# Optimization experiments

Hardware: AMD Instinct MI355X
Metric: run time of the kernel (lower is better)

The kernel has to match this reference:

```python
import math
import jax, jax.numpy as jnp
import numpy as np

B, T, C = 8, 1024, 512
H = 8
NUM_FRAMES = 128  # num_tokens
NUM_ANIMALS = 8   # num_id; NUM_FRAMES * NUM_ANIMALS == T


def _linear_params(key, fan_in, fan_out):
    kw, kb = jax.random.split(key)
    bound = 1.0 / math.sqrt(fan_in)
    W = jax.random.uniform(kw, (fan_out, fan_in), jnp.float32, -bound, bound)
    b = jax.random.uniform(kb, (fan_out,), jnp.float32, -bound, bound)
    return W, b


def setup_inputs() -> dict:
    key = jax.random.key(0)
    ks = jax.random.split(key, 6)
    x = jax.random.normal(ks[0], (B, T, C), jnp.float32)
    mask = jnp.ones((B, T), jnp.float32)
    Wq, bq = _linear_params(ks[1], C, C)
    Wk, bk = _linear_params(ks[2], C, C)
    Wv, bv = _linear_params(ks[3], C, C)
    Wp, bp = _linear_params(ks[4], C, C)
    return {"x": x, "mask": mask, "Wq": Wq, "bq": bq, "Wk": Wk, "bk": bk,
            "Wv": Wv, "bv": bv, "Wp": Wp, "bp": bp}


def _block_causal_mask():
    # tril over frames, expanded so all animals within a frame attend to all
    # animals of frames <= current frame: kron(tril(F,F), ones(I,I)) -> (T,T)
    tril = jnp.tril(jnp.ones((NUM_FRAMES, NUM_FRAMES), jnp.float32))
    return jnp.kron(tril, jnp.ones((NUM_ANIMALS, NUM_ANIMALS), jnp.float32))


def reference(x, mask, Wq, bq, Wk, bk, Wv, bv, Wp, bp):
    Bx, Tx, Cx = x.shape
    d = Cx // H
    q = (x @ Wq.T + bq).reshape(Bx, Tx, H, d).transpose(0, 2, 1, 3)  # b h t d
    k = (x @ Wk.T + bk).reshape(Bx, Tx, H, d).transpose(0, 2, 1, 3)
    v = (x @ Wv.T + bv).reshape(Bx, Tx, H, d).transpose(0, 2, 1, 3)
    att = jnp.einsum('bhqd,bhkd->bhqk', q, k) * (1.0 / math.sqrt(d))
    m = _block_causal_mask()[None, None] * mask[:, None, None, :]  # (B,1,T,T)
    att = jnp.where(m == 0, -jnp.inf, att)
    att = jax.nn.softmax(att, axis=-1)
    # dropout is identity (pdrop=0.0 / eval mode)
    y = jnp.einsum('bhqk,bhkd->bhqd', att, v)
    y = y.transpose(0, 2, 1, 3).reshape(Bx, Tx, Cx)
    return y @ Wp.T + bp
```

## Files before the change

kernel.cpp:

```cpp
#include <hip/hip_runtime.h>
#include <cstdint>
#include <cstddef>

#define BB 8
#define TT 1024
#define CC 512
#define HH 8
#define DD 64
#define MM (BB*TT)

typedef short s16x4 __attribute__((ext_vector_type(4)));
typedef _Float16 f16x8 __attribute__((ext_vector_type(8)));
typedef float f32x4  __attribute__((ext_vector_type(4)));
typedef unsigned u32x4 __attribute__((ext_vector_type(4)));

__device__ __forceinline__ short f2hs(float f) {
  _Float16 h = (_Float16)f;
  return __builtin_bit_cast(short, h);
}
__device__ __forceinline__ unsigned pkh(float a, float b) {
  return __builtin_bit_cast(unsigned, __builtin_amdgcn_cvt_pkrtz(a, b));
}

__device__ __forceinline__ f32x4 mfma16h(f16x8 a, f16x8 b, f32x4 c) {
  return __builtin_amdgcn_mfma_f32_16x16x32_f16(a, b, c, 0, 0, 0);
}

__device__ __forceinline__ void gload_lds16(const void* g, void* l) {
  __builtin_amdgcn_global_load_lds(
      (const __attribute__((address_space(1))) unsigned int*)g,
      (__attribute__((address_space(3))) unsigned int*)l, 16, 0, 0);
}

__global__ void prep_kernel(const float* __restrict__ x,
                            const float* __restrict__ mask,
                            const float* __restrict__ Wq,
                            const float* __restrict__ Wk,
                            const float* __restrict__ Wv,
                            const float* __restrict__ Wp,
                            short* __restrict__ Xh,
                            short* __restrict__ Wqkv,
                            short* __restrict__ Wpc,
                            float* __restrict__ maskAdd) {
  const int NXv = MM * CC / 4;
  const int NWv = CC * CC / 4;
  const int NM = BB * TT;
  int stride = gridDim.x * blockDim.x;
  for (int i = blockIdx.x * blockDim.x + threadIdx.x; i < NXv + 4 * NWv + NM; i += stride) {
    if (i < NXv) {
      int e = i * 4;
      float4 v = *(const float4*)(x + e);
      s16x4 h = {f2hs(v.x), f2hs(v.y), f2hs(v.z), f2hs(v.w)};
      *(s16x4*)(Xh + e) = h;
    } else if (i < NXv + 4 * NWv) {
      int wi = i - NXv;
      int wsel = wi >> 16;
      int idx = wi & 65535;
      int r = idx >> 7, c = (idx & 127) << 2;
      const float* W = (wsel == 0) ? Wq : (wsel == 1) ? Wk : (wsel == 2) ? Wv : Wp;
      float4 v = *(const float4*)(W + (size_t)r * CC + c);
      s16x4 h = {f2hs(v.x), f2hs(v.y), f2hs(v.z), f2hs(v.w)};
      short* dst = (wsel < 3) ? (Wqkv + (size_t)(wsel * 512 + r) * CC + c)
                              : (Wpc + (size_t)r * CC + c);
      *(s16x4*)dst = h;
    } else {
      int mi = i - NXv - 4 * NWv;
      maskAdd[mi] = (mask[mi] == 0.f) ? -1e30f : 0.f;
    }
  }
}

template <int BN, int EPI>
__global__ __launch_bounds__(512, 4) void gemm_kernel(
    const short* __restrict__ A, const short* __restrict__ Bw,
    const float* __restrict__ b0, const float* __restrict__ b1,
    const float* __restrict__ b2,
    short* __restrict__ qo, short* __restrict__ ko, short* __restrict__ vt,
    float* __restrict__ outp) {
  constexpr int MR = 4;
  constexpr int NR = BN / 64;
  constexpr int ABYT = 128 * 128;
  constexpr int TILE = ABYT + BN * 128;
  constexpr int NT = 8;
  constexpr int BL = BN / 64;
  __shared__ __align__(1024) char smem[2 * TILE];

  const int tid = threadIdx.x;
  const int lane = tid & 63;
  const int w = tid >> 6;
  const int wm = w >> 2, wn = w & 3;
  const int l15 = lane & 15, lg = lane >> 4;
  const int lsw = (l15 & 7) << 4;
  const int sr8 = lane >> 3;
  const int scbsw = ((lane & 7) * 16) ^ (sr8 << 4);

  const int rowA = blockIdx.x * 128;
  const int rowB = blockIdx.y * BN;
  const char* Ab = (const char*)A + (size_t)(rowA + sr8) * 1024 + scbsw;
  const char* Bb = (const char*)Bw + (size_t)(rowB + sr8) * 1024 + scbsw;

  f32x4 acc[MR][NR] = {};

  auto STAGE_A = [&](char* dst, int kt) {
#pragma unroll
    for (int g = 0; g < 2; ++g) {
      int r0 = (w * 2 + g) * 8;
      gload_lds16(Ab + (size_t)r0 * 1024 + (size_t)kt * 128, dst + r0 * 128);
    }
  };
  auto STAGE_B = [&](char* dst, int kt) {
#pragma unroll
    for (int g = 0; g < BL; ++g) {
      int r0 = (w * BL + g) * 8;
      gload_lds16(Bb + (size_t)r0 * 1024 + (size_t)kt * 128, dst + ABYT + r0 * 128);
    }
  };
  auto RDA2 = [&](const char* buf, int mh, int kk, f16x8* af) {
#pragma unroll
    for (int i = 0; i < 2; ++i) {
      int row = wm * 64 + (mh * 2 + i) * 16 + l15;
      af[i] = *(const f16x8*)(buf + row * 128 + ((kk * 64 + lg * 16) ^ lsw));
    }
  };
  auto RDBk = [&](const char* buf, int kk, f16x8* bfr) {
#pragma unroll
    for (int j = 0; j < NR; ++j) {
      int row = wn * (BN / 4) + j * 16 + l15;
      bfr[j] = *(const f16x8*)(buf + ABYT + row * 128 + ((kk * 64 + lg * 16) ^ lsw));
    }
  };

  STAGE_A(smem, 0);
  STAGE_B(smem, 0);
  asm volatile("s_waitcnt vmcnt(0)" ::: "memory");
  __builtin_amdgcn_s_barrier();

  for (int t = 0; t < NT; ++t) {
    char* bufp = smem + (t & 1) * TILE;
    char* bufn = smem + ((t + 1) & 1) * TILE;
    f16x8 af[2], bfr[NR];

#define PH(MH)                                                                \
  __builtin_amdgcn_s_barrier();                                               \
  asm volatile("s_waitcnt lgkmcnt(0)" ::: "memory");                          \
  __builtin_amdgcn_sched_barrier(0);                                          \
  __builtin_amdgcn_s_setprio(1);                                              \
  _Pragma("unroll")                                                           \
  for (int i = 0; i < 2; ++i)                                                 \
    _Pragma("unroll")                                                         \
    for (int j = 0; j < NR; ++j)                                              \
      acc[(MH) * 2 + i][j] = mfma16h(af[i], bfr[j], acc[(MH) * 2 + i][j]);    \
  __builtin_amdgcn_s_setprio(0);

    RDBk(bufp, 0, bfr);
    RDA2(bufp, 0, 0, af);
    if (t + 1 < NT) STAGE_A(bufn, t + 1);
    PH(0)
    RDA2(bufp, 1, 0, af);
    if (t + 1 < NT) STAGE_B(bufn, t + 1);
    PH(1)
    RDBk(bufp, 1, bfr);
    RDA2(bufp, 1, 1, af);
    PH(1)
    RDA2(bufp, 0, 1, af);
    PH(0)
#undef PH
    asm volatile("s_waitcnt vmcnt(0)" ::: "memory");
    __builtin_amdgcn_s_barrier();
  }

#pragma unroll
  for (int m = 0; m < MR; ++m) {
    int rbase = rowA + wm * 64 + m * 16 + lg * 4;
#pragma unroll
    for (int n = 0; n < NR; ++n) {
      int col = rowB + wn * (BN / 4) + n * 16 + l15;
#pragma unroll
      for (int j = 0; j < 4; ++j) {
        float v = acc[m][n][j];
        int r = rbase + j;
        if constexpr (EPI == 0) {
          int b = r >> 10, t = r & 1023;
          int wsel = col >> 9, c = col & 511;
          int h = c >> 6, dd = c & 63;
          int bh = b * HH + h;
          if (wsel == 0) {
            qo[((size_t)bh * TT + t) * DD + dd] = f2hs((v + b0[c]) * 0.125f);
          } else if (wsel == 1) {
            ko[((size_t)bh * TT + t) * DD + dd] = f2hs(v + b1[c]);
          } else {
            vt[((size_t)bh * DD + dd) * TT + t] = f2hs(v + b2[c]);
          }
        } else {
          outp[(size_t)r * CC + col] = v + b0[col];
        }
      }
    }
  }
}

__global__ __launch_bounds__(256, 4) void attn_kernel(
    const short* __restrict__ q, const short* __restrict__ k,
    const short* __restrict__ vt, const float* __restrict__ maskAdd,
    short* __restrict__ Yh) {
  const int blk = blockIdx.x;
  const int k4 = blk >> 8;
  const int r = blk & 255;
  const int bh = r >> 2;
  const int j4 = r & 3;
  const int qb = (k4 & 1) ? ((k4 & 2) ? (4 + j4) : j4)
                          : ((k4 & 2) ? (11 - j4) : (15 - j4));
  const int b = bh >> 3, h = bh & 7;
  const int tid = threadIdx.x;
  const int lane = tid & 63;
  const int w = tid >> 6;
  const int l15 = lane & 15, lg = lane >> 4;
  const int lsw = (l15 & 7) << 4;

  __shared__ short Ks[2][64 * 64];
  __shared__ short Vs[2][64 * 64];

  const short* kbh = k + (size_t)bh * TT * DD;
  const short* vbh = vt + (size_t)bh * DD * TT;

  const int sr32 = tid >> 3;
  const int scb = (tid & 7) * 16;

  auto STAGE = [&](int bs, int tile) {
#pragma unroll
    for (int g = 0; g < 2; ++g) {
      int row = g * 32 + sr32;
      int sw = (row & 7) << 4;
      gload_lds16((const char*)kbh + ((size_t)tile * 64 + row) * 128 + (scb ^ sw),
                  (char*)&Ks[bs][0] + row * 128);
      gload_lds16((const char*)vbh + (size_t)row * 2048 + tile * 128 + (scb ^ sw),
                  (char*)&Vs[bs][0] + row * 128);
    }
  };

  const int qrow = qb * 64 + w * 16 + l15;
  const short* qptr = q + ((size_t)bh * TT + qrow) * DD;
  f16x8 qf0 = *(const f16x8*)(qptr + lg * 8);
  f16x8 qf1 = *(const f16x8*)(qptr + 32 + lg * 8);

  f32x4 yacc[4] = {};
  float mrun = -1e30f, lpart = 0.f;

  const int srcA = (((2 * lg) & 3) << 4) + l15;
  const int srcB = (((2 * lg + 1) & 3) << 4) + l15;
  const bool hiSel = (lg >= 2);

  STAGE(0, 0);
  __syncthreads();

  int buf = 0;
  for (int jt = 0; jt <= qb; ++jt) {
    if (jt < qb) STAGE(buf ^ 1, jt + 1);

    f32x4 sacc[4];
#pragma unroll
    for (int n = 0; n < 4; ++n)
      sacc[n] = *(const f32x4*)(maskAdd + (size_t)b * TT + jt * 64 + n * 16 + lg * 4);
    __builtin_amdgcn_s_setprio(1);
#pragma unroll
    for (int c = 0; c < 2; ++c) {
      f16x8 qc = (c == 0) ? qf0 : qf1;
#pragma unroll
      for (int n = 0; n < 4; ++n) {
        int krow = n * 16 + l15;
        const f16x8 kf = *(const f16x8*)((const char*)&Ks[buf][0] + krow * 128 + ((c * 64 + lg * 16) ^ lsw));
        sacc[n] = mfma16h(kf, qc, sacc[n]);
      }
    }
    __builtin_amdgcn_s_setprio(0);
    if (jt == qb) {
      const int qloc8 = (w * 16 + l15) >> 3;
#pragma unroll
      for (int n = 0; n < 4; ++n)
#pragma unroll
        for (int jj = 0; jj < 4; ++jj) {
          int kloc = n * 16 + lg * 4 + jj;
          if ((kloc >> 3) > qloc8) sacc[n][jj] = -1e30f;
        }
    }
    float t0 = fmaxf(fmaxf(sacc[0][0], sacc[0][1]), fmaxf(sacc[0][2], sacc[0][3]));
    float t1 = fmaxf(fmaxf(sacc[1][0], sacc[1][1]), fmaxf(sacc[1][2], sacc[1][3]));
    float t2 = fmaxf(fmaxf(sacc[2][0], sacc[2][1]), fmaxf(sacc[2][2], sacc[2][3]));
    float t3 = fmaxf(fmaxf(sacc[3][0], sacc[3][1]), fmaxf(sacc[3][2], sacc[3][3]));
    float pmL = fmaxf(fmaxf(t0, t1), fmaxf(t2, t3));
    if (!__all(pmL <= mrun + 8.0f)) {
      float pm = fmaxf(pmL, __shfl_xor(pmL, 16));
      pm = fmaxf(pm, __shfl_xor(pm, 32));
      float mnew = fmaxf(mrun, pm);
      float alpha = __expf(mrun - mnew);
      mrun = mnew;
      lpart *= alpha;
      float ab[4];
#pragma unroll
      for (int jj = 0; jj < 4; ++jj) ab[jj] = __shfl(alpha, lg * 4 + jj);
#pragma unroll
      for (int dt = 0; dt < 4; ++dt)
#pragma unroll
        for (int jj = 0; jj < 4; ++jj) yacc[dt][jj] *= ab[jj];
    }
    unsigned pk2[4][2];
    float lps = 0.f;
#pragma unroll
    for (int n = 0; n < 4; ++n) {
      float p0 = __expf(sacc[n][0] - mrun);
      float p1 = __expf(sacc[n][1] - mrun);
      float p2 = __expf(sacc[n][2] - mrun);
      float p3 = __expf(sacc[n][3] - mrun);
      lps += (p0 + p1) + (p2 + p3);
      pk2[n][0] = pkh(p0, p1);
      pk2[n][1] = pkh(p2, p3);
    }
    lpart += lps;
    f16x8 pa[2];
#pragma unroll
    for (int c = 0; c < 2; ++c) {
      unsigned a0 = __shfl(pk2[2 * c][0], srcA);
      unsigned a1 = __shfl(pk2[2 * c][1], srcA);
      unsigned a2 = __shfl(pk2[2 * c][0], srcB);
      unsigned a3 = __shfl(pk2[2 * c][1], srcB);
      unsigned b0 = __shfl(pk2[2 * c + 1][0], srcA);
      unsigned b1 = __shfl(pk2[2 * c + 1][1], srcA);
      unsigned b2 = __shfl(pk2[2 * c + 1][0], srcB);
      unsigned b3 = __shfl(pk2[2 * c + 1][1], srcB);
      u32x4 tv = {hiSel ? b0 : a0, hiSel ? b1 : a1, hiSel ? b2 : a2, hiSel ? b3 : a3};
      pa[c] = __builtin_bit_cast(f16x8, tv);
    }
    __builtin_amdgcn_s_setprio(1);
#pragma unroll
    for (int c = 0; c < 2; ++c) {
#pragma unroll
      for (int dt = 0; dt < 4; ++dt) {
        int vrow = dt * 16 + l15;
        const f16x8 vf = *(const f16x8*)((const char*)&Vs[buf][0] + vrow * 128 + ((c * 64 + lg * 16) ^ lsw));
        yacc[dt] = mfma16h(pa[c], vf, yacc[dt]);
      }
    }
    __builtin_amdgcn_s_setprio(0);

    __syncthreads();
    buf ^= 1;
  }

  float lr = lpart;
  lr += __shfl_xor(lr, 16);
  lr += __shfl_xor(lr, 32);
  float lb[4];
#pragma unroll
  for (int jj = 0; jj < 4; ++jj) lb[jj] = 1.f / __shfl(lr, lg * 4 + jj);
#pragma unroll
  for (int dt = 0; dt < 4; ++dt) {
    int col = h * DD + dt * 16 + l15;
#pragma unroll
    for (int jj = 0; jj < 4; ++jj) {
      int row = b * TT + qb * 64 + w * 16 + lg * 4 + jj;
      float y = yacc[dt][jj] * lb[jj];
      Yh[(size_t)row * CC + col] = f2hs(y);
    }
  }
}

extern "C" void kernel_launch(void* const* d_in, const int* in_sizes, int n_in,
                              void* d_out, int out_size, void* d_ws, size_t ws_size,
                              hipStream_t stream) {
  const float* x    = (const float*)d_in[0];
  const float* mask = (const float*)d_in[1];
  const float* Wq   = (const float*)d_in[2];
  const float* bq   = (const float*)d_in[3];
  const float* Wk   = (const float*)d_in[4];
  const float* bk   = (const float*)d_in[5];
  const float* Wv   = (const float*)d_in[6];
  const float* bv   = (const float*)d_in[7];
  const float* Wp   = (const float*)d_in[8];
  const float* bp   = (const float*)d_in[9];
  float* out = (float*)d_out;

  char* ws = (char*)d_ws;
  short* Xh   = (short*)(ws);
  short* Wqkv = (short*)(ws + (size_t)8 * 1048576);
  short* Wpc  = (short*)(ws + (size_t)10 * 1048576);
  short* qo   = (short*)(ws + (size_t)11 * 1048576);
  short* ko   = (short*)(ws + (size_t)19 * 1048576);
  short* vt   = (short*)(ws + (size_t)27 * 1048576);
  short* Yh   = (short*)(ws + (size_t)35 * 1048576);
  float* maskAdd = (float*)(ws + (size_t)43 * 1048576);

  prep_kernel<<<2048, 256, 0, stream>>>(x, mask, Wq, Wk, Wv, Wp, Xh, Wqkv, Wpc, maskAdd);

  gemm_kernel<192, 0><<<dim3(64, 8), 512, 0, stream>>>(
      Xh, Wqkv, bq, bk, bv, qo, ko, vt, nullptr);

  attn_kernel<<<dim3(1024), 256, 0, stream>>>(qo, ko, vt, maskAdd, Yh);

  gemm_kernel<64, 1><<<dim3(64, 8), 512, 0, stream>>>(
      Yh, Wpc, bp, nullptr, nullptr, nullptr, nullptr, nullptr, out);
}
```

Before: 73.99 us.

## Fuse attention and output projection with grid barrier; retile QKV GEMM

Merges the attention and output-projection kernels into one persistent 512-block kernel. Each block runs two (batch, head) attention units, then all blocks meet at a global atomic barrier before doing the projection GEMM. The QKV GEMM moves to 96-wide N tiles on a 64x16 grid so more blocks run, and the barrier counters are reset in the prep kernel. This removes one kernel launch and the launch gap, but the spin barrier assumes all 512 blocks are resident at once and adds a synchronisation stall.

```diff
diff --git a/kernel.cpp b/kernel.cpp
--- a/kernel.cpp
+++ b/kernel.cpp
@@ -41,7 +41,9 @@
                             short* __restrict__ Xh,
                             short* __restrict__ Wqkv,
                             short* __restrict__ Wpc,
-                            float* __restrict__ maskAdd) {
+                            float* __restrict__ maskAdd,
+                            unsigned* __restrict__ bar) {
+  if (blockIdx.x == 0 && threadIdx.x == 0) { bar[0] = 0u; bar[1] = 0u; }
   const int NXv = MM * CC / 4;
   const int NWv = CC * CC / 4;
   const int NM = BB * TT;
@@ -70,32 +72,29 @@
   }
 }
 
-template <int BN, int EPI>
-__global__ __launch_bounds__(512, 4) void gemm_kernel(
+__global__ __launch_bounds__(512, 4) void qkv_kernel(
     const short* __restrict__ A, const short* __restrict__ Bw,
     const float* __restrict__ b0, const float* __restrict__ b1,
     const float* __restrict__ b2,
-    short* __restrict__ qo, short* __restrict__ ko, short* __restrict__ vt,
-    float* __restrict__ outp) {
-  constexpr int MR = 4;
-  constexpr int NR = BN / 64;
-  constexpr int ABYT = 128 * 128;
-  constexpr int TILE = ABYT + BN * 128;
+    short* __restrict__ qo, short* __restrict__ ko, short* __restrict__ vt) {
+  constexpr int MR = 2, NR = 3;
+  constexpr int ABYT = 16384;
+  constexpr int BBYT = 96 * 128;
+  constexpr int TILE = ABYT + BBYT;
   constexpr int NT = 8;
-  constexpr int BL = BN / 64;
   __shared__ __align__(1024) char smem[2 * TILE];
 
   const int tid = threadIdx.x;
   const int lane = tid & 63;
   const int w = tid >> 6;
-  const int wm = w >> 2, wn = w & 3;
+  const int wm = w >> 1, wn = w & 1;
   const int l15 = lane & 15, lg = lane >> 4;
   const int lsw = (l15 & 7) << 4;
   const int sr8 = lane >> 3;
   const int scbsw = ((lane & 7) * 16) ^ (sr8 << 4);
 
   const int rowA = blockIdx.x * 128;
-  const int rowB = blockIdx.y * BN;
+  const int rowB = blockIdx.y * 96;
   const char* Ab = (const char*)A + (size_t)(rowA + sr8) * 1024 + scbsw;
   const char* Bb = (const char*)Bw + (size_t)(rowB + sr8) * 1024 + scbsw;
 
@@ -109,23 +108,24 @@
     }
   };
   auto STAGE_B = [&](char* dst, int kt) {
-#pragma unroll
-    for (int g = 0; g < BL; ++g) {
-      int r0 = (w * BL + g) * 8;
-      gload_lds16(Bb + (size_t)r0 * 1024 + (size_t)kt * 128, dst + ABYT + r0 * 128);
+    int r0 = w * 8;
+    gload_lds16(Bb + (size_t)r0 * 1024 + (size_t)kt * 128, dst + ABYT + r0 * 128);
+    if (w < 4) {
+      int r1 = (8 + w) * 8;
+      gload_lds16(Bb + (size_t)r1 * 1024 + (size_t)kt * 128, dst + ABYT + r1 * 128);
     }
   };
-  auto RDA2 = [&](const char* buf, int mh, int kk, f16x8* af) {
-#pragma unroll
-    for (int i = 0; i < 2; ++i) {
-      int row = wm * 64 + (mh * 2 + i) * 16 + l15;
+  auto RDA = [&](const char* buf, int kk, f16x8* af) {
+#pragma unroll
+    for (int i = 0; i < MR; ++i) {
+      int row = wm * 32 + i * 16 + l15;
       af[i] = *(const f16x8*)(buf + row * 128 + ((kk * 64 + lg * 16) ^ lsw));
     }
   };
-  auto RDBk = [&](const char* buf, int kk, f16x8* bfr) {
+  auto RDB = [&](const char* buf, int kk, f16x8* bfr) {
 #pragma unroll
     for (int j = 0; j < NR; ++j) {
-      int row = wn * (BN / 4) + j * 16 + l15;
+      int row = wn * 48 + j * 16 + l15;
       bfr[j] = *(const f16x8*)(buf + ABYT + row * 128 + ((kk * 64 + lg * 16) ^ lsw));
     }
   };
@@ -138,228 +138,338 @@
   for (int t = 0; t < NT; ++t) {
     char* bufp = smem + (t & 1) * TILE;
     char* bufn = smem + ((t + 1) & 1) * TILE;
-    f16x8 af[2], bfr[NR];
-
-#define PH(MH)                                                                \
+    f16x8 af[MR], bfr[NR];
+
+    RDB(bufp, 0, bfr);
+    RDA(bufp, 0, af);
+    if (t + 1 < NT) STAGE_A(bufn, t + 1);
+    __builtin_amdgcn_s_barrier();
+    asm volatile("s_waitcnt lgkmcnt(0)" ::: "memory");
+    __builtin_amdgcn_sched_barrier(0);
+    __builtin_amdgcn_s_setprio(1);
+#pragma unroll
+    for (int i = 0; i < MR; ++i)
+#pragma unroll
+      for (int j = 0; j < NR; ++j)
+        acc[i][j] = mfma16h(af[i], bfr[j], acc[i][j]);
+    __builtin_amdgcn_s_setprio(0);
+
+    RDB(bufp, 1, bfr);
+    RDA(bufp, 1, af);
+    if (t + 1 < NT) STAGE_B(bufn, t + 1);
+    __builtin_amdgcn_s_barrier();
+    asm volatile("s_waitcnt lgkmcnt(0)" ::: "memory");
+    __builtin_amdgcn_sched_barrier(0);
+    __builtin_amdgcn_s_setprio(1);
+#pragma unroll
+    for (int i = 0; i < MR; ++i)
+#pragma unroll
+      for (int j = 0; j < NR; ++j)
+        acc[i][j] = mfma16h(af[i], bfr[j], acc[i][j]);
+    __builtin_amdgcn_s_setprio(0);
+
+    asm volatile("s_waitcnt vmcnt(0)" ::: "memory");
+    __builtin_amdgcn_s_barrier();
+  }
+
+#pragma unroll
+  for (int m = 0; m < MR; ++m) {
+    int rbase = rowA + wm * 32 + m * 16 + lg * 4;
+#pragma unroll
+    for (int n = 0; n < NR; ++n) {
+      int col = rowB + wn * 48 + n * 16 + l15;
+#pragma unroll
+      for (int j = 0; j < 4; ++j) {
+        float v = acc[m][n][j];
+        int r = rbase + j;
+        int b = r >> 10, t = r & 1023;
+        int wsel = col >> 9, c = col & 511;
+        int h = c >> 6, dd = c & 63;
+        int bh = b * HH + h;
+        if (wsel == 0) {
+          qo[((size_t)bh * TT + t) * DD + dd] = f2hs((v + b0[c]) * 0.125f);
+        } else if (wsel == 1) {
+          ko[((size_t)bh * TT + t) * DD + dd] = f2hs(v + b1[c]);
+        } else {
+          vt[((size_t)bh * DD + dd) * TT + t] = f2hs(v + b2[c]);
+        }
+      }
+    }
+  }
+}
+
+__global__ __launch_bounds__(512, 4) void attnproj_kernel(
+    const short* __restrict__ q, const short* __restrict__ k,
+    const short* __restrict__ vt, const float* __restrict__ maskAdd,
+    short* __restrict__ Yh, const short* __restrict__ Wpc,
+    const float* __restrict__ bp, float* __restrict__ out,
+    unsigned* __restrict__ bar) {
+  __shared__ __align__(1024) char smem[65536];
+
+  const int blk = blockIdx.x;
+  const int tid = threadIdx.x;
+
+  {
+    const int half = blk >> 8;
+    const int lin = blk & 255;
+    const int qb = half ? (15 - (lin >> 5)) : (lin >> 5);
+    const int bhp = lin & 31;
+    const int w8 = tid >> 6;
+    const int u = w8 >> 2;
+    const int w = w8 & 3;
+    const int bh = bhp * 2 + u;
+    const int b = bh >> 3, h = bh & 7;
+    const int lane = tid & 63;
+    const int l15 = lane & 15, lg = lane >> 4;
+    const int lsw = (l15 & 7) << 4;
+
+    char* KsU = smem + u * 32768;
+
+    const short* kbh = k + (size_t)bh * TT * DD;
+    const short* vbh = vt + (size_t)bh * DD * TT;
+
+    const int utid = tid & 255;
+    const int sr32 = utid >> 3;
+    const int scb = (utid & 7) * 16;
+
+    auto STAGE = [&](int bs, int tile) {
+#pragma unroll
+      for (int g = 0; g < 2; ++g) {
+        int row = g * 32 + sr32;
+        int sw = (row & 7) << 4;
+        gload_lds16((const char*)kbh + ((size_t)tile * 64 + row) * 128 + (scb ^ sw),
+                    KsU + bs * 8192 + row * 128);
+        gload_lds16((const char*)vbh + (size_t)row * 2048 + tile * 128 + (scb ^ sw),
+                    KsU + 16384 + bs * 8192 + row * 128);
+      }
+    };
+
+    const int qrow = qb * 64 + w * 16 + l15;
+    const short* qptr = q + ((size_t)bh * TT + qrow) * DD;
+    f16x8 qf0 = *(const f16x8*)(qptr + lg * 8);
+    f16x8 qf1 = *(const f16x8*)(qptr + 32 + lg * 8);
+
+    f32x4 yacc[4] = {};
+    float mrun = -1e30f, lpart = 0.f;
+
+    const int srcA = (((2 * lg) & 3) << 4) + l15;
+    const int srcB = (((2 * lg + 1) & 3) << 4) + l15;
+    const bool hiSel = (lg >= 2);
+
+    STAGE(0, 0);
+    __syncthreads();
+
+    int buf = 0;
+    for (int jt = 0; jt <= qb; ++jt) {
+      if (jt < qb) STAGE(buf ^ 1, jt + 1);
+
+      f32x4 sacc[4];
+#pragma unroll
+      for (int n = 0; n < 4; ++n)
+        sacc[n] = *(const f32x4*)(maskAdd + (size_t)b * TT + jt * 64 + n * 16 + lg * 4);
+      __builtin_amdgcn_s_setprio(1);
+#pragma unroll
+      for (int c = 0; c < 2; ++c) {
+        f16x8 qc = (c == 0) ? qf0 : qf1;
+#pragma unroll
+        for (int n = 0; n < 4; ++n) {
+          int krow = n * 16 + l15;
+          const f16x8 kf = *(const f16x8*)(KsU + buf * 8192 + krow * 128 + ((c * 64 + lg * 16) ^ lsw));
+          sacc[n] = mfma16h(kf, qc, sacc[n]);
+        }
+      }
+      __builtin_amdgcn_s_setprio(0);
+      if (jt == qb) {
+        const int qloc8 = (w * 16 + l15) >> 3;
+#pragma unroll
+        for (int n = 0; n < 4; ++n)
+#pragma unroll
+          for (int jj = 0; jj < 4; ++jj) {
+            int kloc = n * 16 + lg * 4 + jj;
+            if ((kloc >> 3) > qloc8) sacc[n][jj] = -1e30f;
+          }
+      }
+      float t0 = fmaxf(fmaxf(sacc[0][0], sacc[0][1]), fmaxf(sacc[0][2], sacc[0][3]));
+      float t1 = fmaxf(fmaxf(sacc[1][0], sacc[1][1]), fmaxf(sacc[1][2], sacc[1][3]));
+      float t2 = fmaxf(fmaxf(sacc[2][0], sacc[2][1]), fmaxf(sacc[2][2], sacc[2][3]));
+      float t3 = fmaxf(fmaxf(sacc[3][0], sacc[3][1]), fmaxf(sacc[3][2], sacc[3][3]));
+      float pmL = fmaxf(fmaxf(t0, t1), fmaxf(t2, t3));
+      if (!__all(pmL <= mrun + 8.0f)) {
+        float pm = fmaxf(pmL, __shfl_xor(pmL, 16));
+        pm = fmaxf(pm, __shfl_xor(pm, 32));
+        float mnew = fmaxf(mrun, pm);
+        float alpha = __expf(mrun - mnew);
+        mrun = mnew;
+        lpart *= alpha;
+        float ab[4];
+#pragma unroll
+        for (int jj = 0; jj < 4; ++jj) ab[jj] = __shfl(alpha, lg * 4 + jj);
+#pragma unroll
+        for (int dt = 0; dt < 4; ++dt)
+#pragma unroll
+          for (int jj = 0; jj < 4; ++jj) yacc[dt][jj] *= ab[jj];
+      }
+      unsigned pk2[4][2];
+      float lps = 0.f;
+#pragma unroll
+      for (int n = 0; n < 4; ++n) {
+        float p0 = __expf(sacc[n][0] - mrun);
+        float p1 = __expf(sacc[n][1] - mrun);
+        float p2 = __expf(sacc[n][2] - mrun);
+        float p3 = __expf(sacc[n][3] - mrun);
+        lps += (p0 + p1) + (p2 + p3);
+        pk2[n][0] = pkh(p0, p1);
+        pk2[n][1] = pkh(p2, p3);
+      }
+      lpart += lps;
+      f16x8 pa[2];
+#pragma unroll
+      for (int c = 0; c < 2; ++c) {
+        unsigned a0 = __shfl(pk2[2 * c][0], srcA);
+        unsigned a1 = __shfl(pk2[2 * c][1], srcA);
+        unsigned a2 = __shfl(pk2[2 * c][0], srcB);
+        unsigned a3 = __shfl(pk2[2 * c][1], srcB);
+        unsigned b0 = __shfl(pk2[2 * c + 1][0], srcA);
+        unsigned b1 = __shfl(pk2[2 * c + 1][1], srcA);
+        unsigned b2 = __shfl(pk2[2 * c + 1][0], srcB);
+        unsigned b3 = __shfl(pk2[2 * c + 1][1], srcB);
+        u32x4 tv = {hiSel ? b0 : a0, hiSel ? b1 : a1, hiSel ? b2 : a2, hiSel ? b3 : a3};
+        pa[c] = __builtin_bit_cast(f16x8, tv);
+      }
+      __builtin_amdgcn_s_setprio(1);
+#pragma unroll
+      for (int c = 0; c < 2; ++c) {
+#pragma unroll
+        for (int dt = 0; dt < 4; ++dt) {
+          int vrow = dt * 16 + l15;
+          const f16x8 vf = *(const f16x8*)(KsU + 16384 + buf * 8192 + vrow * 128 + ((c * 64 + lg * 16) ^ lsw));
+          yacc[dt] = mfma16h(pa[c], vf, yacc[dt]);
+        }
+      }
+      __builtin_amdgcn_s_setprio(0);
+
+      __syncthreads();
+      buf ^= 1;
+    }
+
+    float lr = lpart;
+    lr += __shfl_xor(lr, 16);
+    lr += __shfl_xor(lr, 32);
+    float lb[4];
+#pragma unroll
+    for (int jj = 0; jj < 4; ++jj) lb[jj] = 1.f / __shfl(lr, lg * 4 + jj);
+#pragma unroll
+    for (int dt = 0; dt < 4; ++dt) {
+      int col = h * DD + dt * 16 + l15;
+#pragma unroll
+      for (int jj = 0; jj < 4; ++jj) {
+        int row = b * TT + qb * 64 + w * 16 + lg * 4 + jj;
+        float y = yacc[dt][jj] * lb[jj];
+        Yh[(size_t)row * CC + col] = f2hs(y);
+      }
+    }
+  }
+
+  __syncthreads();
+  if (tid == 0) {
+    __threadfence();
+    if (atomicAdd(&bar[0], 1u) == 511u) {
+      atomicAdd(&bar[1], 1u);
+    } else {
+      while (atomicAdd(&bar[1], 0u) == 0u) __builtin_amdgcn_s_sleep(8);
+    }
+    __threadfence();
+  }
+  __syncthreads();
+
+  {
+    constexpr int ABYT = 16384;
+    constexpr int TILE = 24576;
+    constexpr int NT = 8;
+    const int bx = blk & 63, by = blk >> 6;
+    const int lane = tid & 63;
+    const int w = tid >> 6;
+    const int wm = w >> 2, wn = w & 3;
+    const int l15 = lane & 15, lg = lane >> 4;
+    const int lsw = (l15 & 7) << 4;
+    const int sr8 = lane >> 3;
+    const int scbsw = ((lane & 7) * 16) ^ (sr8 << 4);
+
+    const int rowA = bx * 128;
+    const int rowB = by * 64;
+    const char* Ab = (const char*)Yh + (size_t)(rowA + sr8) * 1024 + scbsw;
+    const char* Bb = (const char*)Wpc + (size_t)(rowB + sr8) * 1024 + scbsw;
+
+    f32x4 acc[4] = {};
+
+    auto STAGE_A = [&](char* dst, int kt) {
+#pragma unroll
+      for (int g = 0; g < 2; ++g) {
+        int r0 = (w * 2 + g) * 8;
+        gload_lds16(Ab + (size_t)r0 * 1024 + (size_t)kt * 128, dst + r0 * 128);
+      }
+    };
+    auto STAGE_B = [&](char* dst, int kt) {
+      int r0 = w * 8;
+      gload_lds16(Bb + (size_t)r0 * 1024 + (size_t)kt * 128, dst + ABYT + r0 * 128);
+    };
+    auto RDA2 = [&](const char* buf, int mh, int kk, f16x8* af) {
+#pragma unroll
+      for (int i = 0; i < 2; ++i) {
+        int row = wm * 64 + (mh * 2 + i) * 16 + l15;
+        af[i] = *(const f16x8*)(buf + row * 128 + ((kk * 64 + lg * 16) ^ lsw));
+      }
+    };
+    auto RDB1 = [&](const char* buf, int kk) {
+      int row = wn * 16 + l15;
+      return *(const f16x8*)(buf + ABYT + row * 128 + ((kk * 64 + lg * 16) ^ lsw));
+    };
+
+    STAGE_A(smem, 0);
+    STAGE_B(smem, 0);
+    asm volatile("s_waitcnt vmcnt(0)" ::: "memory");
+    __builtin_amdgcn_s_barrier();
+
+    for (int t = 0; t < NT; ++t) {
+      char* bufp = smem + (t & 1) * TILE;
+      char* bufn = smem + ((t + 1) & 1) * TILE;
+      f16x8 af[2], bfr;
+
+#define PJ(MH)                                                                \
   __builtin_amdgcn_s_barrier();                                               \
   asm volatile("s_waitcnt lgkmcnt(0)" ::: "memory");                          \
   __builtin_amdgcn_sched_barrier(0);                                          \
   __builtin_amdgcn_s_setprio(1);                                              \
   _Pragma("unroll")                                                           \
   for (int i = 0; i < 2; ++i)                                                 \
-    _Pragma("unroll")                                                         \
-    for (int j = 0; j < NR; ++j)                                              \
-      acc[(MH) * 2 + i][j] = mfma16h(af[i], bfr[j], acc[(MH) * 2 + i][j]);    \
+    acc[(MH) * 2 + i] = mfma16h(af[i], bfr, acc[(MH) * 2 + i]);               \
   __builtin_amdgcn_s_setprio(0);
 
-    RDBk(bufp, 0, bfr);
-    RDA2(bufp, 0, 0, af);
-    if (t + 1 < NT) STAGE_A(bufn, t + 1);
-    PH(0)
-    RDA2(bufp, 1, 0, af);
-    if (t + 1 < NT) STAGE_B(bufn, t + 1);
-    PH(1)
-    RDBk(bufp, 1, bfr);
-    RDA2(bufp, 1, 1, af);
-    PH(1)
-    RDA2(bufp, 0, 1, af);
-    PH(0)
-#undef PH
-    asm volatile("s_waitcnt vmcnt(0)" ::: "memory");
-    __builtin_amdgcn_s_barrier();
-  }
-
-#pragma unroll
-  for (int m = 0; m < MR; ++m) {
-    int rbase = rowA + wm * 64 + m * 16 + lg * 4;
-#pragma unroll
-    for (int n = 0; n < NR; ++n) {
-      int col = rowB + wn * (BN / 4) + n * 16 + l15;
+      bfr = RDB1(bufp, 0);
+      RDA2(bufp, 0, 0, af);
+      if (t + 1 < NT) STAGE_A(bufn, t + 1);
+      PJ(0)
+      RDA2(bufp, 1, 0, af);
+      if (t + 1 < NT) STAGE_B(bufn, t + 1);
+      PJ(1)
+      bfr = RDB1(bufp, 1);
+      RDA2(bufp, 1, 1, af);
+      PJ(1)
+      RDA2(bufp, 0, 1, af);
+      PJ(0)
+#undef PJ
+      asm volatile("s_waitcnt vmcnt(0)" ::: "memory");
+      __builtin_amdgcn_s_barrier();
+    }
+
+#pragma unroll
+    for (int m = 0; m < 4; ++m) {
+      int rbase = rowA + wm * 64 + m * 16 + lg * 4;
+      int col = rowB + wn * 16 + l15;
 #pragma unroll
       for (int j = 0; j < 4; ++j) {
-        float v = acc[m][n][j];
-        int r = rbase + j;
-        if constexpr (EPI == 0) {
-          int b = r >> 10, t = r & 1023;
-          int wsel = col >> 9, c = col & 511;
-          int h = c >> 6, dd = c & 63;
-          int bh = b * HH + h;
-          if (wsel == 0) {
-            qo[((size_t)bh * TT + t) * DD + dd] = f2hs((v + b0[c]) * 0.125f);
-          } else if (wsel == 1) {
-            ko[((size_t)bh * TT + t) * DD + dd] = f2hs(v + b1[c]);
-          } else {
-            vt[((size_t)bh * DD + dd) * TT + t] = f2hs(v + b2[c]);
-          }
-        } else {
-          outp[(size_t)r * CC + col] = v + b0[col];
-        }
-      }
-    }
-  }
-}
-
-__global__ __launch_bounds__(256, 4) void attn_kernel(
-    const short* __restrict__ q, const short* __restrict__ k,
-    const short* __restrict__ vt, const float* __restrict__ maskAdd,
-    short* __restrict__ Yh) {
-  const int blk = blockIdx.x;
-  const int k4 = blk >> 8;
-  const int r = blk & 255;
-  const int bh = r >> 2;
-  const int j4 = r & 3;
-  const int qb = (k4 & 1) ? ((k4 & 2) ? (4 + j4) : j4)
-                          : ((k4 & 2) ? (11 - j4) : (15 - j4));
-  const int b = bh >> 3, h = bh & 7;
-  const int tid = threadIdx.x;
-  const int lane = tid & 63;
-  const int w = tid >> 6;
-  const int l15 = lane & 15, lg = lane >> 4;
-  const int lsw = (l15 & 7) << 4;
-
-  __shared__ short Ks[2][64 * 64];
-  __shared__ short Vs[2][64 * 64];
-
-  const short* kbh = k + (size_t)bh * TT * DD;
-  const short* vbh = vt + (size_t)bh * DD * TT;
-
-  const int sr32 = tid >> 3;
-  const int scb = (tid & 7) * 16;
-
-  auto STAGE = [&](int bs, int tile) {
-#pragma unroll
-    for (int g = 0; g < 2; ++g) {
-      int row = g * 32 + sr32;
-      int sw = (row & 7) << 4;
-      gload_lds16((const char*)kbh + ((size_t)tile * 64 + row) * 128 + (scb ^ sw),
-                  (char*)&Ks[bs][0] + row * 128);
-      gload_lds16((const char*)vbh + (size_t)row * 2048 + tile * 128 + (scb ^ sw),
-                  (char*)&Vs[bs][0] + row * 128);
-    }
-  };
-
-  const int qrow = qb * 64 + w * 16 + l15;
-  const short* qptr = q + ((size_t)bh * TT + qrow) * DD;
-  f16x8 qf0 = *(const f16x8*)(qptr + lg * 8);
-  f16x8 qf1 = *(const f16x8*)(qptr + 32 + lg * 8);
-
-  f32x4 yacc[4] = {};
-  float mrun = -1e30f, lpart = 0.f;
-
-  const int srcA = (((2 * lg) & 3) << 4) + l15;
-  const int srcB = (((2 * lg + 1) & 3) << 4) + l15;
-  const bool hiSel = (lg >= 2);
-
-  STAGE(0, 0);
-  __syncthreads();
-
-  int buf = 0;
-  for (int jt = 0; jt <= qb; ++jt) {
-    if (jt < qb) STAGE(buf ^ 1, jt + 1);
-
-    f32x4 sacc[4];
-#pragma unroll
-    for (int n = 0; n < 4; ++n)
-      sacc[n] = *(const f32x4*)(maskAdd + (size_t)b * TT + jt * 64 + n * 16 + lg * 4);
-    __builtin_amdgcn_s_setprio(1);
-#pragma unroll
-    for (int c = 0; c < 2; ++c) {
-      f16x8 qc = (c == 0) ? qf0 : qf1;
-#pragma unroll
-      for (int n = 0; n < 4; ++n) {
-        int krow = n * 16 + l15;
-        const f16x8 kf = *(const f16x8*)((const char*)&Ks[buf][0] + krow * 128 + ((c * 64 + lg * 16) ^ lsw));
-        sacc[n] = mfma16h(kf, qc, sacc[n]);
-      }
-    }
-    __builtin_amdgcn_s_setprio(0);
-    if (jt == qb) {
-      const int qloc8 = (w * 16 + l15) >> 3;
-#pragma unroll
-      for (int n = 0; n < 4; ++n)
-#pragma unroll
-        for (int jj = 0; jj < 4; ++jj) {
-          int kloc = n * 16 + lg * 4 + jj;
-          if ((kloc >> 3) > qloc8) sacc[n][jj] = -1e30f;
-        }
-    }
-    float t0 = fmaxf(fmaxf(sacc[0][0], sacc[0][1]), fmaxf(sacc[0][2], sacc[0][3]));
-    float t1 = fmaxf(fmaxf(sacc[1][0], sacc[1][1]), fmaxf(sacc[1][2], sacc[1][3]));
-    float t2 = fmaxf(fmaxf(sacc[2][0], sacc[2][1]), fmaxf(sacc[2][2], sacc[2][3]));
-    float t3 = fmaxf(fmaxf(sacc[3][0], sacc[3][1]), fmaxf(sacc[3][2], sacc[3][3]));
-    float pmL = fmaxf(fmaxf(t0, t1), fmaxf(t2, t3));
-    if (!__all(pmL <= mrun + 8.0f)) {
-      float pm = fmaxf(pmL, __shfl_xor(pmL, 16));
-      pm = fmaxf(pm, __shfl_xor(pm, 32));
-      float mnew = fmaxf(mrun, pm);
-      float alpha = __expf(mrun - mnew);
-      mrun = mnew;
-      lpart *= alpha;
-      float ab[4];
-#pragma unroll
-      for (int jj = 0; jj < 4; ++jj) ab[jj] = __shfl(alpha, lg * 4 + jj);
-#pragma unroll
-      for (int dt = 0; dt < 4; ++dt)
-#pragma unroll
-        for (int jj = 0; jj < 4; ++jj) yacc[dt][jj] *= ab[jj];
-    }
-    unsigned pk2[4][2];
-    float lps = 0.f;
-#pragma unroll
-    for (int n = 0; n < 4; ++n) {
-      float p0 = __expf(sacc[n][0] - mrun);
-      float p1 = __expf(sacc[n][1] - mrun);
-      float p2 = __expf(sacc[n][2] - mrun);
-      float p3 = __expf(sacc[n][3] - mrun);
-      lps += (p0 + p1) + (p2 + p3);
-      pk2[n][0] = pkh(p0, p1);
-      pk2[n][1] = pkh(p2, p3);
-    }
-    lpart += lps;
-    f16x8 pa[2];
-#pragma unroll
-    for (int c = 0; c < 2; ++c) {
-      unsigned a0 = __shfl(pk2[2 * c][0], srcA);
-      unsigned a1 = __shfl(pk2[2 * c][1], srcA);
-      unsigned a2 = __shfl(pk2[2 * c][0], srcB);
-      unsigned a3 = __shfl(pk2[2 * c][1], srcB);
-      unsigned b0 = __shfl(pk2[2 * c + 1][0], srcA);
-      unsigned b1 = __shfl(pk2[2 * c + 1][1], srcA);
-      unsigned b2 = __shfl(pk2[2 * c + 1][0], srcB);
-      unsigned b3 = __shfl(pk2[2 * c + 1][1], srcB);
-      u32x4 tv = {hiSel ? b0 : a0, hiSel ? b1 : a1, hiSel ? b2 : a2, hiSel ? b3 : a3};
-      pa[c] = __builtin_bit_cast(f16x8, tv);
-    }
-    __builtin_amdgcn_s_setprio(1);
-#pragma unroll
-    for (int c = 0; c < 2; ++c) {
-#pragma unroll
-      for (int dt = 0; dt < 4; ++dt) {
-        int vrow = dt * 16 + l15;
-        const f16x8 vf = *(const f16x8*)((const char*)&Vs[buf][0] + vrow * 128 + ((c * 64 + lg * 16) ^ lsw));
-        yacc[dt] = mfma16h(pa[c], vf, yacc[dt]);
-      }
-    }
-    __builtin_amdgcn_s_setprio(0);
-
-    __syncthreads();
-    buf ^= 1;
-  }
-
-  float lr = lpart;
-  lr += __shfl_xor(lr, 16);
-  lr += __shfl_xor(lr, 32);
-  float lb[4];
-#pragma unroll
-  for (int jj = 0; jj < 4; ++jj) lb[jj] = 1.f / __shfl(lr, lg * 4 + jj);
-#pragma unroll
-  for (int dt = 0; dt < 4; ++dt) {
-    int col = h * DD + dt * 16 + l15;
-#pragma unroll
-    for (int jj = 0; jj < 4; ++jj) {
-      int row = b * TT + qb * 64 + w * 16 + lg * 4 + jj;
-      float y = yacc[dt][jj] * lb[jj];
-      Yh[(size_t)row * CC + col] = f2hs(y);
+        out[(size_t)(rbase + j) * CC + col] = acc[m][j] + bp[col];
+      }
     }
   }
 }
@@ -388,14 +498,14 @@
   short* vt   = (short*)(ws + (size_t)27 * 1048576);
   short* Yh   = (short*)(ws + (size_t)35 * 1048576);
   float* maskAdd = (float*)(ws + (size_t)43 * 1048576);
-
-  prep_kernel<<<2048, 256, 0, stream>>>(x, mask, Wq, Wk, Wv, Wp, Xh, Wqkv, Wpc, maskAdd);
-
-  gemm_kernel<192, 0><<<dim3(64, 8), 512, 0, stream>>>(
-      Xh, Wqkv, bq, bk, bv, qo, ko, vt, nullptr);
-
-  attn_kernel<<<dim3(1024), 256, 0, stream>>>(qo, ko, vt, maskAdd, Yh);
-
-  gemm_kernel<64, 1><<<dim3(64, 8), 512, 0, stream>>>(
-      Yh, Wpc, bp, nullptr, nullptr, nullptr, nullptr, nullptr, out);
-}
+  unsigned* bar  = (unsigned*)(ws + (size_t)44 * 1048576);
+
+  prep_kernel<<<2048, 256, 0, stream>>>(x, mask, Wq, Wk, Wv, Wp, Xh, Wqkv, Wpc,
+                                        maskAdd, bar);
+
+  qkv_kernel<<<dim3(64, 16), 512, 0, stream>>>(
+      Xh, Wqkv, bq, bk, bv, qo, ko, vt);
+
+  attnproj_kernel<<<dim3(512), 512, 0, stream>>>(
+      qo, ko, vt, maskAdd, Yh, Wpc, bp, out, bar);
+}
```

Measured after the change: 138.8 us. +87.6%, slower.
